# Performance work log

Measured on AMD Instinct MI355X. Metric: run time of the kernel, lower is better.

The kernel has to match this reference:

```python
import jax, jax.numpy as jnp
import numpy as np

# --- static configuration (matches init_kwargs) ---
D = 16          # data_dim
H = 128         # hidden_dim
WID = 256       # vf_hidden_dim
LAB = 10        # label_dim
T = 200001      # len(ts) == len(intervals); logsig has T-1 rows
LSIG = 1 + D + D * (D - 1) // 2  # 137, depth-2 log-signature dim
NSTEPS = 100    # heun fixed-step: (ts[-1]-ts[0])/dt0 with dt0=0.01 over [0,1]
II, JJ = np.triu_indices(D, 1)   # depth-2 Hall pairs (i<j), row-major == HallSet order


def setup_inputs() -> dict:
    key = jax.random.key(0)
    ks = jax.random.split(key, 12)
    ts = jnp.linspace(0.0, 1.0, T, dtype=jnp.float32)
    logsig = jax.random.normal(ks[0], (T - 1, LSIG), jnp.float32) * 0.1
    x0 = jax.random.normal(ks[1], (D,), jnp.float32)

    def lin(kw, kb, fan_in, fan_out):
        bnd = 1.0 / np.sqrt(fan_in)
        w = jax.random.uniform(kw, (fan_in, fan_out), jnp.float32, -bnd, bnd)
        b = jax.random.uniform(kb, (fan_out,), jnp.float32, -bnd, bnd)
        return w, b

    l1_w, l1_b = lin(ks[2], ks[3], D, H)          # linear1: data_dim -> hidden
    w1, b1 = lin(ks[4], ks[5], H, WID)            # vf MLP layer 1
    w2, b2 = lin(ks[6], ks[7], WID, WID)          # vf MLP layer 2
    w3, b3 = lin(ks[8], ks[9], WID, D * H)        # vf MLP output layer
    l2_w, l2_b = lin(ks[10], ks[11], H, LAB)      # linear2: hidden -> label
    return dict(ts=ts, logsig=logsig, x0=x0, intervals=ts,
                l1_w=l1_w, l1_b=l1_b, w1=w1, b1=b1, w2=w2, b2=b2,
                w3=w3, b3=b3, l2_w=l2_w, l2_b=l2_b)


def reference(ts, logsig, x0, intervals, l1_w, l1_b, w1, b1, w2, b2, w3, b3, l2_w, l2_b):
    def mlp(y):  # VectorField: silu hidden layers, tanh final, scale=1
        h1 = jax.nn.silu(y @ w1 + b1)
        h2 = jax.nn.silu(h1 @ w2 + b2)
        return jnp.tanh(h2 @ w3 + b3)  # (D*H,)

    def field(t, y):
        # locate the log-signature interval containing t
        idx = jnp.clip(jnp.searchsorted(intervals[1:], t) + 1, 1, T - 1)
        ls = logsig[idx - 1]                       # (LSIG,)
        # primal + linearization of the vector field (forward-mode JVPs)
        vf_out, f_jvp = jax.linearize(mlp, y)
        W = vf_out.reshape(D, H)                   # vf directions, one per channel
        jvps = jax.vmap(f_jvp)(W).reshape(D, D, H) # jvps[k,i,:] = d vf_i / dy . W_k
        lie = jvps[II, JJ] - jvps[JJ, II]          # (D*(D-1)/2, H) Lie brackets
        res = ls[1:D + 1] @ W + ls[D + 1:] @ lie   # linear + bracket terms
        return res / (intervals[idx] - intervals[idx - 1])

    y0 = x0 @ l1_w + l1_b                          # linear1
    dt = (ts[-1] - ts[0]) / NSTEPS                 # fixed-step heun grid

    def step(carry, _):
        t, y = carry
        k1 = field(t, y)
        k2 = field(t + dt, y + dt * k1)
        return (t + dt, y + 0.5 * dt * (k1 + k2)), None

    (_, yT), _ = jax.lax.scan(step, (ts[0], y0), None, length=NSTEPS)
    return jax.nn.softmax(yT @ l2_w + l2_b, axis=-1)  # classification head
```

## Files before the change

kernel.cpp:

```cpp
#include <hip/hip_runtime.h>
#include <math.h>

#define AGENT __HIP_MEMORY_SCOPE_AGENT

constexpr int kNWG   = 32;
constexpr int kTPB   = 256;
constexpr int kD     = 16;
constexpr int kH     = 128;
constexpr int kW     = 256;
constexpr int kOut   = 2048;
constexpr int kLsig  = 137;
constexpr int kT     = 200001;
constexpr int kNRow  = 101;
constexpr int kNEval = 200;

constexpr int FLAGS_OFF = 0;
constexpr int IDX_OFF   = 32;
constexpr int INV_OFF   = 160;
constexpr int YB_OFF    = 288;
constexpr int H1B_OFF   = 416;
constexpr int H2B_OFF   = 672;
constexpr int WB_OFF    = 928;
constexpr int T1B_OFF   = 2976;
constexpr int T2B_OFF   = 7072;
constexpr int RSP_OFF   = 11168;

__device__ __forceinline__ float b2f(unsigned short u){
  union { unsigned int i; float f; } v; v.i = ((unsigned int)u) << 16; return v.f;
}
__device__ __forceinline__ unsigned short f2b(float f){
  unsigned int x = __float_as_uint(f);
  unsigned int r = x + 0x7fffu + ((x >> 16) & 1u);
  return (unsigned short)(r >> 16);
}
__device__ __forceinline__ float ldf(const void* p, size_t i, bool bf){
  return bf ? b2f(((const unsigned short*)p)[i]) : ((const float*)p)[i];
}
__device__ __forceinline__ float aload(const float* p){
  return __hip_atomic_load(p, __ATOMIC_RELAXED, AGENT);
}
__device__ __forceinline__ void astore(float* p, float v){
  __hip_atomic_store(p, v, __ATOMIC_RELAXED, AGENT);
}
__device__ __forceinline__ int pairidx(int i, int j){
  return i*15 - (i*(i-1))/2 + (j - i - 1);
}

__device__ __forceinline__ void gbar(unsigned* flags, int g, unsigned epoch, int tid){
  asm volatile("s_waitcnt vmcnt(0)" ::: "memory");
  __syncthreads();
  if (tid == 0)
    __hip_atomic_store(&flags[g], epoch, __ATOMIC_RELAXED, AGENT);
  if (tid < kNWG){
    int spins = 0;
    while (__hip_atomic_load(&flags[tid], __ATOMIC_RELAXED, AGENT) < epoch){
      __builtin_amdgcn_s_sleep(1);
      if (++spins > (1 << 16)) break;
    }
  }
  __syncthreads();
}

__global__ void cde_init(const void* __restrict__ tsp, const void* __restrict__ x0p,
                         const void* __restrict__ l1wp, const void* __restrict__ l1bp,
                         float* __restrict__ ws)
{
  const int tid = threadIdx.x;
  const bool bf = (((const unsigned*)tsp)[0] != 0u);
  const float ts0 = ldf(tsp, 0, bf);
  const float dt  = (ldf(tsp, kT-1, bf) - ts0) / 100.0f;

  if (tid < kNWG) ((unsigned*)(ws + FLAGS_OFF))[tid] = 0u;

  if (tid < kNRow){
    float t = ts0;
    for (int i = 0; i < tid; i++) t += dt;
    const int N1 = kT - 1;
    int lo = 0, hi = N1;
    while (lo < hi){
      int mid = (lo + hi) >> 1;
      if (ldf(tsp, 1 + mid, bf) < t) lo = mid + 1; else hi = mid;
    }
    int idx = lo + 1; if (idx > kT-1) idx = kT-1; if (idx < 1) idx = 1;
    ((int*)ws)[IDX_OFF + tid] = idx;
    float w = ldf(tsp, idx, bf) - ldf(tsp, idx-1, bf);
    ws[INV_OFF + tid] = (w > 0.f) ? (1.0f / w) : 0.f;
  }
  if (tid < kH){
    float acc = ldf(l1bp, tid, bf);
    for (int d2 = 0; d2 < kD; d2++) acc += ldf(x0p, d2, bf) * ldf(l1wp, d2*kH + tid, bf);
    ws[YB_OFF + tid] = acc;
  }
}

struct SMem {
  float w3T[64][257];
  float w1cT[8][129];
  float w2cT[8][257];
  float Wt[kD][129];
  float T1[kD][257];
  float h1[kW], h2[kW];
  float ls[kLsig + 7];
  float y[kH], ymid[kH], k1v[kH];
  float Urow[kW];
  float red[4][64];
  float tanhp[64];
  float s1p[8], s2p[8], b1c[8], b2c[8];
  float b3c[64];
  float Acol[kD];
  float lgts[16];
};
static_assert(sizeof(SMem) <= 120*1024, "LDS budget");

__global__ __launch_bounds__(kTPB, 1)
void cde_main(const void* __restrict__ tsp, const void* __restrict__ logsigp,
              const void* __restrict__ w1p, const void* __restrict__ b1p,
              const void* __restrict__ w2p, const void* __restrict__ b2p,
              const void* __restrict__ w3p, const void* __restrict__ b3p,
              const void* __restrict__ l2wp, const void* __restrict__ l2bp,
              float* __restrict__ ws, void* __restrict__ outp)
{
  __shared__ SMem s;
  const int g = blockIdx.x, tid = threadIdx.x;
  const int lane = tid & 63, wave = tid >> 6;
  const bool bf = (((const unsigned*)tsp)[0] != 0u);
  unsigned* flags = (unsigned*)(ws + FLAGS_OFF);
  float* h1b = ws + H1B_OFF;  float* h2b = ws + H2B_OFF;
  float* Wb  = ws + WB_OFF;   float* T1b = ws + T1B_OFF;
  float* T2b = ws + T2B_OFF;  float* rsp = ws + RSP_OFF;

  for (int i = tid; i < 8*kH; i += kTPB){ int o = i>>7, j = i&127; s.w1cT[o][j] = ldf(w1p, (size_t)j*kW + g*8 + o, bf); }
  for (int i = tid; i < 8*kW; i += kTPB){ int o = i>>8, n = i&255; s.w2cT[o][n] = ldf(w2p, (size_t)n*kW + g*8 + o, bf); }
  for (int i = tid; i < 64*kW; i += kTPB){ int n = i>>6, c = i&63;  s.w3T[c][n]  = ldf(w3p, (size_t)n*kOut + g*64 + c, bf); }
  if (tid < 8){ s.b1c[tid] = ldf(b1p, g*8 + tid, bf); s.b2c[tid] = ldf(b2p, g*8 + tid, bf); }
  if (tid < 64) s.b3c[tid] = ldf(b3p, g*64 + tid, bf);
  if (tid < kH) s.y[tid] = ws[YB_OFF + tid];
  const float dt  = (ldf(tsp, kT-1, bf) - ldf(tsp, 0, bf)) / 100.0f;
  const float dth = 0.5f * dt;
  __syncthreads();

  unsigned epoch = 0;

  for (int e = 0; e < kNEval; e++){
    const int r = (e + 1) >> 1;
    {
      const int idx = ((const int*)ws)[IDX_OFF + r];
      const float inv = ws[INV_OFF + r];
      for (int c = tid; c < kLsig; c += kTPB)
        s.ls[c] = ldf(logsigp, (size_t)(idx - 1)*kLsig + c, bf) * inv;
    }
    __syncthreads();
    const float* ycur = (e & 1) ? s.ymid : s.y;

    {
      const int o = tid >> 5, l = tid & 31;
      float acc = 0.f;
      #pragma unroll
      for (int jj = 0; jj < 4; jj++){ int j = jj*32 + l; acc += ycur[j] * s.w1cT[o][j]; }
      #pragma unroll
      for (int off = 16; off; off >>= 1) acc += __shfl_down(acc, off, 32);
      if (l == 0){
        float z = acc + s.b1c[o];
        float sg = 1.0f / (1.0f + expf(-z));
        s.s1p[o] = sg * (1.0f + z*(1.0f - sg));
        astore(h1b + g*8 + o, z * sg);
      }
    }
    gbar(flags, g, ++epoch, tid);
    s.h1[tid] = aload(h1b + tid);
    __syncthreads();

    {
      const int o = tid >> 5, l = tid & 31;
      float acc = 0.f;
      #pragma unroll
      for (int jj = 0; jj < 8; jj++){ int j = jj*32 + l; acc += s.h1[j] * s.w2cT[o][j]; }
      #pragma unroll
      for (int off = 16; off; off >>= 1) acc += __shfl_down(acc, off, 32);
      if (l == 0){
        float z = acc + s.b2c[o];
        float sg = 1.0f / (1.0f + expf(-z));
        s.s2p[o] = sg * (1.0f + z*(1.0f - sg));
        astore(h2b + g*8 + o, z * sg);
      }
    }
    gbar(flags, g, ++epoch, tid);
    s.h2[tid] = aload(h2b + tid);
    __syncthreads();

    {
      float acc = 0.f;
      #pragma unroll 8
      for (int j = 0; j < 64; j++) acc += s.h2[wave*64 + j] * s.w3T[lane][wave*64 + j];
      s.red[wave][lane] = acc;
    }
    __syncthreads();
    if (wave == 0){
      float z3 = s.red[0][lane] + s.red[1][lane] + s.red[2][lane] + s.red[3][lane] + s.b3c[lane];
      float Wv = tanhf(z3);
      s.tanhp[lane] = 1.0f - Wv*Wv;
      astore(Wb + g*64 + lane, Wv);
    }
    gbar(flags, g, ++epoch, tid);
    for (int i = tid; i < kD*kH; i += kTPB){ int k = i>>7, h = i&127; s.Wt[k][h] = aload(Wb + i); }
    __syncthreads();

    {
      const int outi = tid >> 1, half = tid & 1;
      const int k = outi >> 3, o = outi & 7;
      float acc = 0.f;
      #pragma unroll
      for (int jj = 0; jj < 64; jj++){ int j = jj*2 + half; acc += s.Wt[k][j] * s.w1cT[o][j]; }
      acc += __shfl_xor(acc, 1);
      if (half == 0) astore(T1b + k*kW + g*8 + o, acc * s.s1p[o]);
    }
    gbar(flags, g, ++epoch, tid);
    for (int i = tid; i < kD*kW; i += kTPB){ int k = i>>8, n = i&255; s.T1[k][n] = aload(T1b + i); }
    __syncthreads();

    {
      const int outi = tid >> 1, half = tid & 1;
      const int k = outi >> 3, o = outi & 7;
      float acc = 0.f;
      #pragma unroll 16
      for (int jj = 0; jj < 128; jj++){ int n = jj*2 + half; acc += s.T1[k][n] * s.w2cT[o][n]; }
      acc += __shfl_xor(acc, 1);
      if (half == 0) astore(T2b + k*kW + g*8 + o, acc * s.s2p[o]);
    }
    gbar(flags, g, ++epoch, tid);

    if (tid < kD){
      const int ig = g >> 1; const int k = tid; float v = 0.f;
      if (k < ig)      v =  s.ls[17 + pairidx(k, ig)];
      else if (k > ig) v = -s.ls[17 + pairidx(ig, k)];
      s.Acol[k] = v;
    }
    __syncthreads();
    {
      float u = 0.f; const int n = tid;
      #pragma unroll
      for (int k2 = 0; k2 < kD; k2++) u += s.Acol[k2] * aload(T2b + k2*kW + n);
      s.Urow[n] = u;
    }
    __syncthreads();
    {
      float acc = 0.f;
      #pragma unroll 8
      for (int j = 0; j < 64; j++) acc += s.Urow[wave*64 + j] * s.w3T[lane][wave*64 + j];
      s.red[wave][lane] = acc;
    }
    __syncthreads();
    if (wave == 0){
      float v = (s.red[0][lane] + s.red[1][lane] + s.red[2][lane] + s.red[3][lane]) * s.tanhp[lane];
      if (g < 2){
        float lin = 0.f; const int h = g*64 + lane;
        #pragma unroll
        for (int k2 = 0; k2 < kD; k2++) lin += s.ls[1 + k2] * s.Wt[k2][h];
        v += lin;
      }
      astore(rsp + g*64 + lane, v);
    }
    gbar(flags, g, ++epoch, tid);

    if (tid < kH){
      const int hh = tid >> 6, hl = tid & 63;
      float rs = 0.f;
      #pragma unroll
      for (int i2 = 0; i2 < kD; i2++) rs += aload(rsp + (2*i2 + hh)*64 + hl);
      if (!(e & 1)){ s.k1v[tid] = rs; s.ymid[tid] = s.y[tid] + dt * rs; }
      else         { s.y[tid] = s.y[tid] + dth * (s.k1v[tid] + rs); }
    }
    __syncthreads();
  }

  if (g == 0){
    if (tid < 10){
      float acc = ldf(l2bp, tid, bf);
      for (int h = 0; h < kH; h++) acc += s.y[h] * ldf(l2wp, (size_t)h*10 + tid, bf);
      s.lgts[tid] = acc;
    }
    __syncthreads();
    if (tid < 10){
      float m = s.lgts[0];
      #pragma unroll
      for (int i2 = 1; i2 < 10; i2++) m = fmaxf(m, s.lgts[i2]);
      float num = expf(s.lgts[tid] - m);
      float den = 0.f;
      #pragma unroll
      for (int i2 = 0; i2 < 10; i2++) den += expf(s.lgts[i2] - m);
      float v = num / den;
      if (bf) ((unsigned short*)outp)[tid] = f2b(v);
      else    ((float*)outp)[tid] = v;
    }
  }
}

extern "C" void kernel_launch(void* const* d_in, const int* in_sizes, int n_in,
                              void* d_out, int out_size, void* d_ws, size_t ws_size,
                              hipStream_t stream)
{
  const void* ts   = d_in[0];
  const void* lsig = d_in[1];
  const void* x0   = d_in[2];
  const void* l1w  = d_in[4];
  const void* l1b  = d_in[5];
  const void* w1   = d_in[6];
  const void* b1   = d_in[7];
  const void* w2   = d_in[8];
  const void* b2   = d_in[9];
  const void* w3   = d_in[10];
  const void* b3   = d_in[11];
  const void* l2w  = d_in[12];
  const void* l2b  = d_in[13];
  float* ws = (float*)d_ws;

  hipLaunchKernelGGL(cde_init, dim3(1), dim3(128), 0, stream, ts, x0, l1w, l1b, ws);
  hipLaunchKernelGGL(cde_main, dim3(kNWG), dim3(kTPB), 0, stream,
                     ts, lsig, w1, b1, w2, b2, w3, b3, l2w, l2b, ws, d_out);
}
```

Measured before the change: 4.801 ms.

## Replace grid barriers for h1/h2 exchange with tagged 64-bit value polling

The two grid-wide barriers after the first and second MLP layers are replaced by per-element 64-bit slots that pack an evaluation tag with the value. Each consumer thread polls its own slot until the tag matches, so no separate flag barrier round-trip is needed. This removes a store-fence-flag-poll sequence twice per evaluation, in exchange for per-element spin loops and a reliance on relaxed atomics, with no ordering guarantee beyond the tag itself.

```diff
diff --git a/kernel.cpp b/kernel.cpp
--- a/kernel.cpp
+++ b/kernel.cpp
@@ -13,17 +13,18 @@
 constexpr int kT     = 200001;
 constexpr int kNRow  = 101;
 constexpr int kNEval = 200;
+constexpr int SPIN_MAX = 1 << 16;
 
 constexpr int FLAGS_OFF = 0;
 constexpr int IDX_OFF   = 32;
 constexpr int INV_OFF   = 160;
 constexpr int YB_OFF    = 288;
-constexpr int H1B_OFF   = 416;
-constexpr int H2B_OFF   = 672;
 constexpr int WB_OFF    = 928;
 constexpr int T1B_OFF   = 2976;
 constexpr int T2B_OFF   = 7072;
 constexpr int RSP_OFF   = 11168;
+constexpr int H1T_U64   = 6608;
+constexpr int H2T_U64   = 6864;
 
 __device__ __forceinline__ float b2f(unsigned short u){
   union { unsigned int i; float f; } v; v.i = ((unsigned int)u) << 16; return v.f;
@@ -41,6 +42,15 @@
 }
 __device__ __forceinline__ void astore(float* p, float v){
   __hip_atomic_store(p, v, __ATOMIC_RELAXED, AGENT);
+}
+__device__ __forceinline__ unsigned long long aload64(const unsigned long long* p){
+  return __hip_atomic_load(p, __ATOMIC_RELAXED, AGENT);
+}
+__device__ __forceinline__ void astore64(unsigned long long* p, unsigned long long v){
+  __hip_atomic_store(p, v, __ATOMIC_RELAXED, AGENT);
+}
+__device__ __forceinline__ unsigned long long pk64(unsigned tag, float f){
+  return ((unsigned long long)tag << 32) | (unsigned long long)__float_as_uint(f);
 }
 __device__ __forceinline__ int pairidx(int i, int j){
   return i*15 - (i*(i-1))/2 + (j - i - 1);
@@ -55,7 +65,7 @@
     int spins = 0;
     while (__hip_atomic_load(&flags[tid], __ATOMIC_RELAXED, AGENT) < epoch){
       __builtin_amdgcn_s_sleep(1);
-      if (++spins > (1 << 16)) break;
+      if (++spins > SPIN_MAX) break;
     }
   }
   __syncthreads();
@@ -71,6 +81,10 @@
   const float dt  = (ldf(tsp, kT-1, bf) - ts0) / 100.0f;
 
   if (tid < kNWG) ((unsigned*)(ws + FLAGS_OFF))[tid] = 0u;
+  {
+    unsigned long long* tg = ((unsigned long long*)ws) + H1T_U64;
+    for (int i = tid; i < 512; i += 128) tg[i] = 0ULL;
+  }
 
   if (tid < kNRow){
     float t = ts0;
@@ -125,9 +139,10 @@
   const int lane = tid & 63, wave = tid >> 6;
   const bool bf = (((const unsigned*)tsp)[0] != 0u);
   unsigned* flags = (unsigned*)(ws + FLAGS_OFF);
-  float* h1b = ws + H1B_OFF;  float* h2b = ws + H2B_OFF;
   float* Wb  = ws + WB_OFF;   float* T1b = ws + T1B_OFF;
   float* T2b = ws + T2B_OFF;  float* rsp = ws + RSP_OFF;
+  unsigned long long* h1t = ((unsigned long long*)ws) + H1T_U64;
+  unsigned long long* h2t = ((unsigned long long*)ws) + H2T_U64;
 
   for (int i = tid; i < 8*kH; i += kTPB){ int o = i>>7, j = i&127; s.w1cT[o][j] = ldf(w1p, (size_t)j*kW + g*8 + o, bf); }
   for (int i = tid; i < 8*kW; i += kTPB){ int o = i>>8, n = i&255; s.w2cT[o][n] = ldf(w2p, (size_t)n*kW + g*8 + o, bf); }
@@ -142,6 +157,7 @@
   unsigned epoch = 0;
 
   for (int e = 0; e < kNEval; e++){
+    const unsigned tag = (unsigned)(e + 1);
     const int r = (e + 1) >> 1;
     {
       const int idx = ((const int*)ws)[IDX_OFF + r];
@@ -163,11 +179,19 @@
         float z = acc + s.b1c[o];
         float sg = 1.0f / (1.0f + expf(-z));
         s.s1p[o] = sg * (1.0f + z*(1.0f - sg));
-        astore(h1b + g*8 + o, z * sg);
-      }
-    }
-    gbar(flags, g, ++epoch, tid);
-    s.h1[tid] = aload(h1b + tid);
+        astore64(h1t + g*8 + o, pk64(tag, z * sg));
+      }
+    }
+    {
+      unsigned long long v = aload64(h1t + tid);
+      int sp = 0;
+      while ((unsigned)(v >> 32) != tag){
+        __builtin_amdgcn_s_sleep(1);
+        v = aload64(h1t + tid);
+        if (++sp > SPIN_MAX) break;
+      }
+      s.h1[tid] = __uint_as_float((unsigned)v);
+    }
     __syncthreads();
 
     {
@@ -181,11 +205,19 @@
         float z = acc + s.b2c[o];
         float sg = 1.0f / (1.0f + expf(-z));
         s.s2p[o] = sg * (1.0f + z*(1.0f - sg));
-        astore(h2b + g*8 + o, z * sg);
-      }
-    }
-    gbar(flags, g, ++epoch, tid);
-    s.h2[tid] = aload(h2b + tid);
+        astore64(h2t + g*8 + o, pk64(tag, z * sg));
+      }
+    }
+    {
+      unsigned long long v = aload64(h2t + tid);
+      int sp = 0;
+      while ((unsigned)(v >> 32) != tag){
+        __builtin_amdgcn_s_sleep(1);
+        v = aload64(h2t + tid);
+        if (++sp > SPIN_MAX) break;
+      }
+      s.h2[tid] = __uint_as_float((unsigned)v);
+    }
     __syncthreads();
 
     {
```

Result: faster. 4.691 ms, median of 2 (-2.3%).
